# Kernel tuning notes

Measured on AMD Instinct MI355X. Metric: run time of the kernel, lower is better.

Reference implementation:

```python
import jax, jax.numpy as jnp
import numpy as np

B, S, L, D = 16, 16, 128, 768   # batch, num_sentences, max_sentence_length, hidden_size
A, T = 8, 5                      # num_args, max_arg_length
VOCAB = 500                      # small id range so arg tokens actually match


def setup_inputs() -> dict:
    key = jax.random.key(0)
    k0, k1, k2, k3, k4, k5 = jax.random.split(key, 6)
    hidden_states = jax.random.normal(k0, (B, S, L, D), dtype=jnp.float32)
    sentence_ids = jax.random.randint(k1, (B, S, L), 0, VOCAB, dtype=jnp.int64)
    # realistic attention masks: ones on a prefix of each sentence
    lens = jax.random.randint(k2, (B, S, 1), L // 2, L + 1)
    sentence_attention_masks = (jnp.arange(L)[None, None, :] < lens).astype(jnp.int32)
    predicate_ids = jax.random.randint(k3, (B, S, A, T), 0, VOCAB, dtype=jnp.int64)
    arg0_ids = jax.random.randint(k4, (B, S, A, T), 0, VOCAB, dtype=jnp.int64)
    arg1_ids = jax.random.randint(k5, (B, S, A, T), 0, VOCAB, dtype=jnp.int64)
    return {
        "hidden_states": hidden_states,
        "sentence_ids": sentence_ids,
        "sentence_attention_masks": sentence_attention_masks,
        "predicate_ids": predicate_ids,
        "arg0_ids": arg0_ids,
        "arg1_ids": arg1_ids,
    }


def _arg_embedding(arg_ids, sentence_ids, hidden):
    # match[b,s,a,t,l] = (sentence token l equals arg token t)
    match = sentence_ids[:, :, None, None, :] == arg_ids[..., None]          # [B,S,A,T,L] bool
    counts = match.sum(-1)                                                   # [B,S,A,T]
    matchf = match.astype(hidden.dtype)
    # per-arg-token mean over matching sentence positions
    avg = jnp.einsum('bsatl,bsld->bsatd', matchf, hidden)
    avg = avg / jnp.maximum(counts, 1).astype(hidden.dtype)[..., None]       # [B,S,A,T,D]
    # torch loop overwrites per token -> keep LAST nonzero token with a match
    valid = (arg_ids != 0) & (counts > 0)                                    # [B,S,A,T]
    Tn = arg_ids.shape[-1]
    last = Tn - 1 - jnp.argmax(valid[..., ::-1].astype(jnp.int32), axis=-1)  # [B,S,A]
    gathered = jnp.take_along_axis(avg, last[..., None, None], axis=3)[..., 0, :]
    return jnp.where(valid.any(-1)[..., None], gathered, jnp.zeros((), hidden.dtype))


def reference(hidden_states, sentence_ids, sentence_attention_masks,
              predicate_ids, arg0_ids, arg1_ids):
    # mean pooling over valid tokens
    m = sentence_attention_masks.astype(hidden_states.dtype)                 # [B,S,L]
    summed = jnp.einsum('bsl,bsld->bsd', m, hidden_states)
    counts = jnp.maximum(m.sum(-1, keepdims=True), 1.0)
    sentence_embeddings_avg = summed / counts                                # [B,S,D]
    predicate_embeddings = _arg_embedding(predicate_ids, sentence_ids, hidden_states)
    arg0_embeddings = _arg_embedding(arg0_ids, sentence_ids, hidden_states)
    arg1_embeddings = _arg_embedding(arg1_ids, sentence_ids, hidden_states)
    return (sentence_embeddings_avg, predicate_embeddings, arg0_embeddings, arg1_embeddings)
```

## Files before the change

### kernel.cpp

```cpp
#include <hip/hip_runtime.h>


namespace {
constexpr int Bc = 16, Sc = 16, Lc = 128, Dc = 768, Ac = 8, Tc = 5;
constexpr int NF4    = Dc / 4;
constexpr int CHUNK  = 32;
constexpr int NCHUNK = NF4 / CHUNK;
constexpr int BLOCK  = 512;
constexpr int RP     = BLOCK / CHUNK;
constexpr int NSLOT  = 3 * Ac;
constexpr int OUT1   = Bc * Sc * NF4;
constexpr int OUTG   = Bc * Sc * Ac * NF4;
}

__global__ __launch_bounds__(BLOCK) void srl_fused(
    const float4* __restrict__ hid,
    const int*    __restrict__ sids,
    const int*    __restrict__ amask,
    const int*    __restrict__ pids,
    const int*    __restrict__ a0ids,
    const int*    __restrict__ a1ids,
    float4*       __restrict__ out)
{
  const int c   = blockIdx.x;
  const int bs  = blockIdx.y;
  const int tid = threadIdx.x;
  const int q   = tid & (CHUNK - 1);
  const int r   = tid >> 5;

  __shared__ int    sid[Lc];
  __shared__ short  slist[NSLOT][Lc];
  __shared__ int    scnt[NSLOT];
  __shared__ float4 red[BLOCK];

  int mval = 0;
  if (tid < Lc) {
    sid[tid] = sids[bs * Lc + tid];
    mval     = amask[bs * Lc + tid];
  }
  const int len = __syncthreads_count(mval != 0);

  const float4* __restrict__ hrow = hid + (size_t)bs * Lc * NF4 + c * CHUNK;

  if (tid < NSLOT) {
    const int g = tid / Ac, a = tid % Ac;
    const int* ids = (g == 0 ? pids : (g == 1 ? a0ids : a1ids)) + (bs * Ac + a) * Tc;
    int tok[Tc], cnt[Tc];
#pragma unroll
    for (int t = 0; t < Tc; ++t) { tok[t] = ids[t]; cnt[t] = 0; }
    for (int l = 0; l < Lc; ++l) {
      const int v = sid[l];
#pragma unroll
      for (int t = 0; t < Tc; ++t) cnt[t] += (v == tok[t]) ? 1 : 0;
    }
    int sel = 0, n = 0;
#pragma unroll
    for (int t = Tc - 1; t >= 0; --t) {
      if (n == 0 && tok[t] != 0 && cnt[t] > 0) { sel = tok[t]; n = cnt[t]; }
    }
    scnt[tid] = n;
    if (n > 0) {
      int k = 0;
      for (int l = 0; l < Lc; ++l)
        if (sid[l] == sel) slist[tid][k++] = (short)l;
    }
  }

  float ax = 0.f, ay = 0.f, az = 0.f, aw = 0.f;
#pragma unroll 4
  for (int l = r; l < len; l += RP) {
    const float4 v = hrow[l * NF4 + q];
    ax += v.x; ay += v.y; az += v.z; aw += v.w;
  }
  red[tid] = make_float4(ax, ay, az, aw);
  __syncthreads();

  if (tid < CHUNK) {
    float4 s = red[q];
#pragma unroll
    for (int p = 1; p < RP; ++p) {
      const float4 t = red[p * CHUNK + q];
      s.x += t.x; s.y += t.y; s.z += t.z; s.w += t.w;
    }
    const float inv = 1.0f / (float)(len > 0 ? len : 1);
    s.x *= inv; s.y *= inv; s.z *= inv; s.w *= inv;
    out[bs * NF4 + c * CHUNK + q] = s;
  }

  for (int j = r; j < NSLOT; j += RP) {
    const int n = scnt[j];
    float ox = 0.f, oy = 0.f, oz = 0.f, ow = 0.f;
    if (n > 0) {
      for (int i = 0; i < n; ++i) {
        const int l = (int)slist[j][i];
        const float4 v = hrow[l * NF4 + q];
        ox += v.x; oy += v.y; oz += v.z; ow += v.w;
      }
      const float inv = 1.0f / (float)n;
      ox *= inv; oy *= inv; oz *= inv; ow *= inv;
    }
    const int g = j / Ac, a = j - g * Ac;
    out[OUT1 + g * OUTG + (bs * Ac + a) * NF4 + c * CHUNK + q] =
        make_float4(ox, oy, oz, ow);
  }
}

extern "C" void kernel_launch(void* const* d_in, const int* in_sizes, int n_in,
                              void* d_out, int out_size, void* d_ws, size_t ws_size,
                              hipStream_t stream) {
  const float4* hid   = (const float4*)d_in[0];
  const int*    sids  = (const int*)d_in[1];
  const int*    amask = (const int*)d_in[2];
  const int*    pids  = (const int*)d_in[3];
  const int*    a0ids = (const int*)d_in[4];
  const int*    a1ids = (const int*)d_in[5];
  float4*       out   = (float4*)d_out;

  srl_fused<<<dim3(NCHUNK, Bc * Sc), dim3(BLOCK), 0, stream>>>(
      hid, sids, amask, pids, a0ids, a1ids, out);
}
```

Before: 166.8 us.

## Split token matching into a prep kernel and shrink main reduction blocks

Moves the per-sentence token counting and match-list construction into a separate prep kernel that runs once per sentence. Before, every column-chunk block redid this serial 24-thread scan. The lists are built in parallel with shared atomics and stored in workspace as byte indices. The main kernel now uses 256-thread blocks over 16-float4 chunks, doubling the grid. The cost is a second launch plus global round-trips for the lengths, counts and lists. Atomic ordering of list entries can change the float summation order.

Measured after the change: 171.5 us. 1.03x slower.

```diff
diff --git a/kernel.cpp b/kernel.cpp
--- a/kernel.cpp
+++ b/kernel.cpp
@@ -4,43 +4,37 @@
 namespace {
 constexpr int Bc = 16, Sc = 16, Lc = 128, Dc = 768, Ac = 8, Tc = 5;
 constexpr int NF4    = Dc / 4;
-constexpr int CHUNK  = 32;
+constexpr int CHUNK  = 16;
 constexpr int NCHUNK = NF4 / CHUNK;
-constexpr int BLOCK  = 512;
+constexpr int BLOCK  = 256;
 constexpr int RP     = BLOCK / CHUNK;
 constexpr int NSLOT  = 3 * Ac;
 constexpr int OUT1   = Bc * Sc * NF4;
 constexpr int OUTG   = Bc * Sc * Ac * NF4;
+constexpr int NBS    = Bc * Sc;
 }
 
-__global__ __launch_bounds__(BLOCK) void srl_fused(
-    const float4* __restrict__ hid,
-    const int*    __restrict__ sids,
-    const int*    __restrict__ amask,
-    const int*    __restrict__ pids,
-    const int*    __restrict__ a0ids,
-    const int*    __restrict__ a1ids,
-    float4*       __restrict__ out)
+__global__ __launch_bounds__(Lc) void srl_prep(
+    const int* __restrict__ sids,
+    const int* __restrict__ amask,
+    const int* __restrict__ pids,
+    const int* __restrict__ a0ids,
+    const int* __restrict__ a1ids,
+    int*           __restrict__ wlen,
+    int*           __restrict__ wscnt,
+    unsigned char* __restrict__ wslist)
 {
-  const int c   = blockIdx.x;
-  const int bs  = blockIdx.y;
+  const int bs  = blockIdx.x;
   const int tid = threadIdx.x;
-  const int q   = tid & (CHUNK - 1);
-  const int r   = tid >> 5;
 
-  __shared__ int    sid[Lc];
-  __shared__ short  slist[NSLOT][Lc];
-  __shared__ int    scnt[NSLOT];
-  __shared__ float4 red[BLOCK];
+  __shared__ int sid[Lc];
+  __shared__ int seltok[NSLOT];
+  __shared__ int cur[NSLOT];
 
-  int mval = 0;
-  if (tid < Lc) {
-    sid[tid] = sids[bs * Lc + tid];
-    mval     = amask[bs * Lc + tid];
-  }
-  const int len = __syncthreads_count(mval != 0);
-
-  const float4* __restrict__ hrow = hid + (size_t)bs * Lc * NF4 + c * CHUNK;
+  sid[tid] = sids[bs * Lc + tid];
+  const int mval = amask[bs * Lc + tid];
+  const int len  = __syncthreads_count(mval != 0);
+  if (tid == 0) wlen[bs] = len;
 
   if (tid < NSLOT) {
     const int g = tid / Ac, a = tid % Ac;
@@ -53,21 +47,47 @@
 #pragma unroll
       for (int t = 0; t < Tc; ++t) cnt[t] += (v == tok[t]) ? 1 : 0;
     }
-    int sel = 0, n = 0;
+    int sel = -1, n = 0;
 #pragma unroll
     for (int t = Tc - 1; t >= 0; --t) {
       if (n == 0 && tok[t] != 0 && cnt[t] > 0) { sel = tok[t]; n = cnt[t]; }
     }
-    scnt[tid] = n;
-    if (n > 0) {
-      int k = 0;
-      for (int l = 0; l < Lc; ++l)
-        if (sid[l] == sel) slist[tid][k++] = (short)l;
+    wscnt[bs * NSLOT + tid] = n;
+    seltok[tid] = (n > 0) ? sel : -1;
+    cur[tid]    = 0;
+  }
+  __syncthreads();
+
+  const int v = sid[tid];
+#pragma unroll
+  for (int j = 0; j < NSLOT; ++j) {
+    if (v == seltok[j]) {
+      const int p = atomicAdd(&cur[j], 1);
+      wslist[(bs * NSLOT + j) * Lc + p] = (unsigned char)tid;
     }
   }
+}
+
+__global__ __launch_bounds__(BLOCK) void srl_main(
+    const float4* __restrict__ hid,
+    const int*           __restrict__ wlen,
+    const int*           __restrict__ wscnt,
+    const unsigned char* __restrict__ wslist,
+    float4*       __restrict__ out)
+{
+  const int c   = blockIdx.x;
+  const int bs  = blockIdx.y;
+  const int tid = threadIdx.x;
+  const int q   = tid & (CHUNK - 1);
+  const int r   = tid >> 4;
+
+  __shared__ float4 red[BLOCK];
+
+  const int len = wlen[bs];
+  const float4* __restrict__ hrow = hid + (size_t)bs * Lc * NF4 + c * CHUNK;
 
   float ax = 0.f, ay = 0.f, az = 0.f, aw = 0.f;
-#pragma unroll 4
+#pragma unroll 2
   for (int l = r; l < len; l += RP) {
     const float4 v = hrow[l * NF4 + q];
     ax += v.x; ay += v.y; az += v.z; aw += v.w;
@@ -76,23 +96,24 @@
   __syncthreads();
 
   if (tid < CHUNK) {
-    float4 s = red[q];
+    float4 s = red[tid];
 #pragma unroll
     for (int p = 1; p < RP; ++p) {
-      const float4 t = red[p * CHUNK + q];
+      const float4 t = red[p * CHUNK + tid];
       s.x += t.x; s.y += t.y; s.z += t.z; s.w += t.w;
     }
     const float inv = 1.0f / (float)(len > 0 ? len : 1);
     s.x *= inv; s.y *= inv; s.z *= inv; s.w *= inv;
-    out[bs * NF4 + c * CHUNK + q] = s;
+    out[bs * NF4 + c * CHUNK + tid] = s;
   }
 
   for (int j = r; j < NSLOT; j += RP) {
-    const int n = scnt[j];
+    const int n = wscnt[bs * NSLOT + j];
     float ox = 0.f, oy = 0.f, oz = 0.f, ow = 0.f;
     if (n > 0) {
+      const unsigned char* lst = wslist + (bs * NSLOT + j) * Lc;
       for (int i = 0; i < n; ++i) {
-        const int l = (int)slist[j][i];
+        const int l = (int)lst[i];
         const float4 v = hrow[l * NF4 + q];
         ox += v.x; oy += v.y; oz += v.z; ow += v.w;
       }
@@ -116,6 +137,12 @@
   const int*    a1ids = (const int*)d_in[5];
   float4*       out   = (float4*)d_out;
 
-  srl_fused<<<dim3(NCHUNK, Bc * Sc), dim3(BLOCK), 0, stream>>>(
-      hid, sids, amask, pids, a0ids, a1ids, out);
+  int*           wlen   = (int*)d_ws;
+  int*           wscnt  = wlen + NBS;
+  unsigned char* wslist = (unsigned char*)(wscnt + NBS * NSLOT);
+
+  srl_prep<<<dim3(NBS), dim3(Lc), 0, stream>>>(
+      sids, amask, pids, a0ids, a1ids, wlen, wscnt, wslist);
+  srl_main<<<dim3(NCHUNK, NBS), dim3(BLOCK), 0, stream>>>(
+      hid, wlen, wscnt, wslist, out);
 }
```
